# Kernel optimization log

Hardware: AMD Instinct MI355X
Metric: run time of the kernel (lower is better)

## Reference

```python
import jax, jax.numpy as jnp
from jax import lax
import numpy as np

B, DIM, NH, H, W = 4, 256, 8, 32, 32
HEAD_DIM = DIM // NH          # 32
KEY_DIM = HEAD_DIM // 2       # attn_ratio = 0.5 -> 16
QKV_OUT = DIM + 2 * NH * KEY_DIM  # 512
SCALE = KEY_DIM ** -0.5


def setup_inputs() -> dict:
    key = jax.random.key(0)
    ks = jax.random.split(key, 11)
    w = lambda k, shape, s=0.05: jax.random.normal(k, shape, jnp.float32) * s
    return {
        "x": jax.random.normal(ks[0], (B, DIM, H, W), jnp.float32),
        "qkv_w": w(ks[1], (QKV_OUT, DIM)),
        "qkv_b": w(ks[2], (QKV_OUT,)),
        "proj_w": w(ks[3], (DIM, DIM)),
        "proj_b": w(ks[4], (DIM,)),
        "pe_w": w(ks[5], (DIM, 1, 3, 3)),
        "pe_b": w(ks[6], (DIM,)),
        "g1_w": w(ks[7], (DIM // 2, DIM)),
        "g1_b": w(ks[8], (DIM // 2,)),
        "g2_w": w(ks[9], (1, DIM // 2)),
        "g2_b": w(ks[10], (1,)),
    }


def conv1x1(x, w, b):
    # fused Conv2d(1x1, bias=False)+BN -> pointwise matmul + bias
    return jnp.einsum('bchw,oc->bohw', x, w) + b[None, :, None, None]


def reference(x, qkv_w, qkv_b, proj_w, proj_b, pe_w, pe_b, g1_w, g1_b, g2_w, g2_b):
    Bx, C, Hh, Ww = x.shape
    N = Hh * Ww
    qkv = conv1x1(x, qkv_w, qkv_b).reshape(Bx, NH, 2 * KEY_DIM + HEAD_DIM, N)
    q = qkv[:, :, :KEY_DIM]                   # [B, nh, key_dim, N]
    k = qkv[:, :, KEY_DIM:2 * KEY_DIM]        # [B, nh, key_dim, N]
    v = qkv[:, :, 2 * KEY_DIM:]               # [B, nh, head_dim, N]

    # attn = q^T @ k * scale  -> [B, nh, N, N]
    attn = jnp.einsum('bhdn,bhdm->bhnm', q, k) * SCALE

    # learned gate -> scalar dynamic k = floor(N * mean(sigmoid(...)))
    g = jax.nn.sigmoid(conv1x1(jax.nn.relu(conv1x1(x, g1_w, g1_b)), g2_w, g2_b))
    dyn_k = jnp.floor(N * jnp.mean(g)).astype(jnp.int32)

    # rank-based top-k mask (jit-friendly equivalent of topk+scatter):
    # keep entries whose descending rank along the last dim is < dyn_k
    order = jnp.argsort(-attn, axis=-1)       # positions sorted by score desc
    ranks = jnp.argsort(order, axis=-1)       # rank of each position
    attn = jnp.where(ranks < dyn_k, attn, -jnp.inf)
    attn = jax.nn.softmax(attn, axis=-1)

    out = jnp.einsum('bhdn,bhmn->bhdm', v, attn).reshape(Bx, C, Hh, Ww)

    # depthwise 3x3 positional-encoding conv on v reshaped to the image grid
    v_img = v.reshape(Bx, C, Hh, Ww)
    pe = lax.conv_general_dilated(
        v_img, pe_w, window_strides=(1, 1), padding=((1, 1), (1, 1)),
        dimension_numbers=('NCHW', 'OIHW', 'NCHW'), feature_group_count=C,
    ) + pe_b[None, :, None, None]

    return conv1x1(out + pe, proj_w, proj_b)
```

## Files before the change

### kernel.cpp

```cpp
#include <hip/hip_runtime.h>
#include <math.h>

#define NTOK 1024
#define CAP 64

#define LDS_FENCE() asm volatile("s_waitcnt lgkmcnt(0)" ::: "memory")

typedef __bf16 bf16x8 __attribute__((ext_vector_type(8)));
typedef unsigned short u16x8 __attribute__((ext_vector_type(8)));
typedef unsigned short u16x4 __attribute__((ext_vector_type(4)));
typedef float f32x4 __attribute__((ext_vector_type(4)));

__device__ __forceinline__ unsigned short f2bf(float f) {
  unsigned int u = __float_as_uint(f);
  return (unsigned short)((u + 0x7fffu + ((u >> 16) & 1u)) >> 16);
}


template<int OC, int OCB, int P, bool RELU, bool VCAST>
__device__ __forceinline__ void conv_body(const float* __restrict__ in,
    const float* __restrict__ w, const float* __restrict__ bias, float* __restrict__ out,
    unsigned short* __restrict__ vbf, int bid, int tid) {
  constexpr int PB = NTOK / (256 * P);
  const int pb = bid % PB; bid /= PB;
  const int ocb = bid % (OC / OCB); const int b = bid / (OC / OCB);
  const int p0 = pb * 256 * P + tid * P;
  const float* inb = in + (size_t)b * 256 * NTOK + p0;
  const float* wrow = w + (size_t)ocb * OCB * 256;

  float acc[OCB][P];
  #pragma unroll
  for (int j = 0; j < OCB; j++)
    #pragma unroll
    for (int i = 0; i < P; i++) acc[j][i] = 0.f;

  #pragma unroll 2
  for (int c0 = 0; c0 < 256; c0 += 4) {
    float4 wl[OCB];
    #pragma unroll
    for (int j = 0; j < OCB; j++) wl[j] = *(const float4*)&wrow[j * 256 + c0];
    #pragma unroll
    for (int cc = 0; cc < 4; cc++) {
      float xr[P];
      if constexpr (P == 4) {
        float4 t = *(const float4*)&inb[(size_t)(c0 + cc) * NTOK];
        xr[0] = t.x; xr[1] = t.y; xr[2] = t.z; xr[3] = t.w;
      } else if constexpr (P == 2) {
        float2 t = *(const float2*)&inb[(size_t)(c0 + cc) * NTOK];
        xr[0] = t.x; xr[1] = t.y;
      } else {
        xr[0] = inb[(size_t)(c0 + cc) * NTOK];
      }
      #pragma unroll
      for (int j = 0; j < OCB; j++) {
        const float wjc = ((const float*)&wl[j])[cc];
        #pragma unroll
        for (int i = 0; i < P; i++) acc[j][i] = fmaf(wjc, xr[i], acc[j][i]);
      }
    }
  }
  #pragma unroll
  for (int j = 0; j < OCB; j++) {
    const int oc = ocb * OCB + j;
    const float bv = bias[oc];
    float r[P];
    #pragma unroll
    for (int i = 0; i < P; i++) {
      float v = acc[j][i] + bv;
      if (RELU) v = fmaxf(v, 0.f);
      r[i] = v;
    }
    float* op = out + ((size_t)b * OC + oc) * NTOK + p0;
    if constexpr (P == 4) *(float4*)op = make_float4(r[0], r[1], r[2], r[3]);
    else if constexpr (P == 2) *(float2*)op = make_float2(r[0], r[1]);
    else *op = r[0];
    if constexpr (VCAST) {
      if ((oc & 63) >= 32) {
        const int c = (oc >> 6) * 32 + (oc & 63) - 32;
        unsigned short* vp = vbf + ((size_t)b * 256 + c) * NTOK + p0;
        #pragma unroll
        for (int i = 0; i < P; i++) vp[i] = f2bf(r[i]);
      }
    }
  }
}

template<int OC, int OCB, int P, bool RELU, bool VCAST>
__global__ __launch_bounds__(256) void conv1x1_kernel(const float* __restrict__ in,
    const float* __restrict__ w, const float* __restrict__ bias, float* __restrict__ out,
    unsigned short* __restrict__ vbf) {
  conv_body<OC, OCB, P, RELU, VCAST>(in, w, bias, out, vbf, blockIdx.x, threadIdx.x);
}

__global__ __launch_bounds__(256) void qkv_gate1_kernel(const float* __restrict__ x,
    const float* __restrict__ qkv_w, const float* __restrict__ qkv_b, float* __restrict__ qkvb,
    unsigned short* __restrict__ vbf,
    const float* __restrict__ g1_w, const float* __restrict__ g1_b, float* __restrict__ gx) {
  const int bid = blockIdx.x;
  if (bid < 512)
    conv_body<512, 8, 2, false, true>(x, qkv_w, qkv_b, qkvb, vbf, bid, threadIdx.x);
  else
    conv_body<128, 8, 2, true, false>(x, g1_w, g1_b, gx, nullptr, bid - 512, threadIdx.x);
}

__global__ __launch_bounds__(256) void gate2_kernel(const float* __restrict__ gx,
    const float* __restrict__ g2_w, const float* __restrict__ g2_b, double* __restrict__ part) {
  const int idx = blockIdx.x * 256 + threadIdx.x;
  const int b = idx >> 10, p = idx & 1023;
  float acc = g2_b[0];
  const float* gb = gx + (size_t)b * 128 * NTOK + p;
  #pragma unroll 4
  for (int j = 0; j < 128; j++) acc = fmaf(g2_w[j], gb[(size_t)j * NTOK], acc);
  float g = 1.f / (1.f + expf(-acc));
  __shared__ double red[256];
  red[threadIdx.x] = (double)g;
  __syncthreads();
  for (int s = 128; s > 0; s >>= 1) {
    if (threadIdx.x < s) red[threadIdx.x] += red[threadIdx.x + s];
    __syncthreads();
  }
  if (threadIdx.x == 0) part[blockIdx.x] = red[0];
}

__global__ __launch_bounds__(512) void attn_kernel(const float* __restrict__ qkv,
    const unsigned short* __restrict__ vbf,
    const double* __restrict__ part, float* __restrict__ out_attn) {
  const int tid = threadIdx.x;
  const int lane = tid & 63, wv = tid >> 6;
  int bid = blockIdx.x;
  const int mb = bid & 127; bid >>= 7;
  const int h = bid & 7; const int b = bid >> 3;

  double dsum = 0.0;
  #pragma unroll
  for (int i = 0; i < 16; i++) dsum += part[i];
  int dk = (int)floor(1024.0 * (dsum / 4096.0));
  const int dyn_k = dk < 1 ? 1 : (dk > NTOK ? NTOK : dk);

  const float* base = qkv + (size_t)(b * 512 + h * 64) * NTOK;

  __shared__ union RowU { float f[1028]; unsigned short pa[1032]; } rows[8];
  __shared__ float invs[8];
  __shared__ union UU {
    struct {
      int hist[8][64];
      int cnt[8];
      float Bv[8]; int Bn[8];
      struct { float v; int n; } cand[8][CAP];
    } sel;
    float pvred[2][4][8][17];
  } u;

  {
    const float2* k2 = (const float2*)(base + 16 * NTOK);
    const float* qb = base + mb * 8;
    float a0[8], a1[8];
    #pragma unroll
    for (int r = 0; r < 8; r++) { a0[r] = 0.f; a1[r] = 0.f; }
    #pragma unroll
    for (int d = 0; d < 16; d++) {
      float2 kk = k2[d * 512 + tid];
      #pragma unroll
      for (int r = 0; r < 8; r++) {
        const float qv = qb[(size_t)d * NTOK + r];
        a0[r] = fmaf(qv, kk.x, a0[r]);
        a1[r] = fmaf(qv, kk.y, a1[r]);
      }
    }
    #pragma unroll
    for (int r = 0; r < 8; r++)
      ((float2*)rows[r].f)[tid] = make_float2(a0[r] * 0.25f, a1[r] * 0.25f);
  }
  __syncthreads();

  {
    const int r = wv;
    float* smrow = rows[r].f;
    float v[16];
    {
      float4 f0 = ((const float4*)smrow)[lane];
      float4 f1 = ((const float4*)smrow)[64 + lane];
      float4 f2 = ((const float4*)smrow)[128 + lane];
      float4 f3 = ((const float4*)smrow)[192 + lane];
      v[0]=f0.x; v[1]=f0.y; v[2]=f0.z; v[3]=f0.w;
      v[4]=f1.x; v[5]=f1.y; v[6]=f1.z; v[7]=f1.w;
      v[8]=f2.x; v[9]=f2.y; v[10]=f2.z; v[11]=f2.w;
      v[12]=f3.x; v[13]=f3.y; v[14]=f3.z; v[15]=f3.w;
    }
    float mn = v[0], mx = v[0];
    #pragma unroll
    for (int i = 1; i < 16; i++) { mn = fminf(mn, v[i]); mx = fmaxf(mx, v[i]); }
    #pragma unroll
    for (int off = 32; off > 0; off >>= 1) {
      mn = fminf(mn, __shfl_xor(mn, off));
      mx = fmaxf(mx, __shfl_xor(mx, off));
    }

    unsigned int keepmask = 0xFFFFu;
    if (dyn_k < NTOK) {
      float Bv = mx; int Bn = dyn_k - 1;
      const float range = mx - mn;
      const bool fine = (range > 0.f);
      int m = 0;
      if (fine) {
        const float s1 = 64.0f / range;
        u.sel.hist[wv][lane] = 0;
        LDS_FENCE();
        int idx1[16];
        #pragma unroll
        for (int i = 0; i < 16; i++) {
          int ix = (int)((v[i] - mn) * s1);
          ix = ix < 0 ? 0 : (ix > 63 ? 63 : ix);
          idx1[i] = ix;
          atomicAdd(&u.sel.hist[wv][ix], 1);
        }
        LDS_FENCE();
        int cum = u.sel.hist[wv][lane];
        #pragma unroll
        for (int off = 1; off < 64; off <<= 1) {
          int o = __shfl_down(cum, off);
          if (lane + off < 64) cum += o;
        }
        int cumNext = __shfl_down(cum, 1);
        if (lane == 63) cumNext = 0;
        unsigned long long bal = __ballot(cum >= dyn_k && cumNext < dyn_k);
        const int t = (int)__builtin_ctzll(bal);
        const int k2 = dyn_k - __shfl(cumNext, t);
        const float binw = range * (1.0f / 64.0f);
        const float lo = mn + (float)t * binw;
        float s2 = 4096.0f / range;
        if (!(s2 < 3.0e38f)) s2 = 0.f;
        u.sel.hist[wv][lane] = 0;
        LDS_FENCE();
        #pragma unroll
        for (int i = 0; i < 16; i++) {
          if (idx1[i] == t) {
            int ix = (int)((v[i] - lo) * s2);
            ix = ix < 0 ? 0 : (ix > 63 ? 63 : ix);
            atomicAdd(&u.sel.hist[wv][ix], 1);
          }
        }
        LDS_FENCE();
        cum = u.sel.hist[wv][lane];
        #pragma unroll
        for (int off = 1; off < 64; off <<= 1) {
          int o = __shfl_down(cum, off);
          if (lane + off < 64) cum += o;
        }
        cumNext = __shfl_down(cum, 1);
        if (lane == 63) cumNext = 0;
        bal = __ballot(cum >= k2 && cumNext < k2);
        const int t2 = (int)__builtin_ctzll(bal);
        const int k3 = k2 - __shfl(cumNext, t2);
        if (lane == 0) u.sel.cnt[wv] = 0;
        LDS_FENCE();
        #pragma unroll
        for (int i = 0; i < 16; i++) {
          if (idx1[i] == t) {
            int ix = (int)((v[i] - lo) * s2);
            ix = ix < 0 ? 0 : (ix > 63 ? 63 : ix);
            if (ix == t2) {
              int p = atomicAdd(&u.sel.cnt[wv], 1);
              if (p < CAP) { u.sel.cand[wv][p].v = v[i]; u.sel.cand[wv][p].n = (i >> 2) * 256 + lane * 4 + (i & 3); }
            }
          }
        }
        LDS_FENCE();
        m = u.sel.cnt[wv];
        if (m <= CAP) {
          for (int ii = lane; ii < m; ii += 64) {
            float cv = u.sel.cand[wv][ii].v; int cn = u.sel.cand[wv][ii].n;
            int rk = 0;
            for (int j = 0; j < m; j++) {
              float ov = u.sel.cand[wv][j].v; int on = u.sel.cand[wv][j].n;
              rk += ((ov > cv) || (ov == cv && on < cn)) ? 1 : 0;
            }
            if (rk == k3 - 1) { u.sel.Bv[wv] = cv; u.sel.Bn[wv] = cn; }
          }
          LDS_FENCE();
          Bv = u.sel.Bv[wv]; Bn = u.sel.Bn[wv];
        }
      }
      if (fine && m > CAP) {
        keepmask = 0u;
        #pragma unroll
        for (int i = 0; i < 16; i++) {
          const int n_i = (i >> 2) * 256 + lane * 4 + (i & 3);
          const float vi = v[i];
          int rk = 0;
          for (int j = 0; j < NTOK; j++) {
            float ov = smrow[j];
            rk += ((ov > vi) || (ov == vi && j < n_i)) ? 1 : 0;
          }
          if (rk < dyn_k) keepmask |= (1u << i);
        }
      } else {
        keepmask = 0u;
        #pragma unroll
        for (int i = 0; i < 16; i++) {
          const int n_i = (i >> 2) * 256 + lane * 4 + (i & 3);
          if ((v[i] > Bv) || (v[i] == Bv && n_i <= Bn)) keepmask |= (1u << i);
        }
      }
    }
    float e[16]; float s = 0.f;
    #pragma unroll
    for (int i = 0; i < 16; i++) {
      e[i] = ((keepmask >> i) & 1u) ? __expf(v[i] - mx) : 0.f;
      s += e[i];
    }
    #pragma unroll
    for (int off = 32; off > 0; off >>= 1) s += __shfl_xor(s, off);
    if (lane == 0) invs[r] = 1.f / s;
    #pragma unroll
    for (int j = 0; j < 4; j++) {
      u16x4 w4 = { f2bf(e[4*j]), f2bf(e[4*j+1]), f2bf(e[4*j+2]), f2bf(e[4*j+3]) };
      *(u16x4*)&rows[r].pa[j * 256 + lane * 4] = w4;
    }
  }
  __syncthreads();

  {
    const int g = lane >> 4;
    const int m16 = lane & 15;
    const int ksl = wv & 3, dt = wv >> 2;
    const unsigned short* vrow = vbf + ((size_t)(b * 256 + h * 32 + dt * 16 + m16)) * NTOK;
    const unsigned short* parow = rows[lane & 7].pa;
    f32x4 acc = {0.f, 0.f, 0.f, 0.f};
    const int nb = ksl * 256;
    #pragma unroll
    for (int ks = 0; ks < 8; ks++) {
      const int n0 = nb + ks * 32 + g * 8;
      bf16x8 a  = __builtin_bit_cast(bf16x8, *(const u16x8*)&parow[n0]);
      bf16x8 b0 = __builtin_bit_cast(bf16x8, *(const u16x8*)&vrow[n0]);
      acc = __builtin_amdgcn_mfma_f32_16x16x32_bf16(a, b0, acc, 0, 0, 0);
    }
    if (g < 2) {
      #pragma unroll
      for (int q = 0; q < 4; q++)
        u.pvred[dt][ksl][g * 4 + q][m16] = acc[q];
    }
  }
  __syncthreads();
  if (tid < 256) {
    const int r2 = tid & 7, d2 = tid >> 3;
    const int dt = d2 >> 4, m16 = d2 & 15;
    float s = u.pvred[dt][0][r2][m16] + u.pvred[dt][1][r2][m16]
            + u.pvred[dt][2][r2][m16] + u.pvred[dt][3][r2][m16];
    s *= invs[r2];
    out_attn[(size_t)(b * 256 + h * 32 + d2) * NTOK + mb * 8 + r2] = s;
  }
}

__global__ __launch_bounds__(256) void pe_kernel(const float* __restrict__ qkv,
    const float* __restrict__ oattn, const float* __restrict__ pe_w,
    const float* __restrict__ pe_b, float* __restrict__ tmp) {
  int bid = blockIdx.x;
  const int c = bid & 255; const int b = bid >> 8;
  const int oc = ((c >> 5) * 64) + 32 + (c & 31);
  const float* vimg = qkv + (size_t)(b * 512 + oc) * NTOK;
  float wloc[9];
  #pragma unroll
  for (int i = 0; i < 9; i++) wloc[i] = pe_w[c * 9 + i];
  const float bv = pe_b[c];
  const int t = threadIdx.x;
  const int p0 = t * 4;
  const int y = p0 >> 5, x0 = p0 & 31;
  float win[3][6];
  #pragma unroll
  for (int dy = -1; dy <= 1; dy++) {
    const int yy = y + dy;
    float* wr = win[dy + 1];
    if (yy < 0 || yy > 31) {
      #pragma unroll
      for (int i = 0; i < 6; i++) wr[i] = 0.f;
    } else {
      const float* vr = vimg + yy * 32;
      wr[0] = (x0 > 0) ? vr[x0 - 1] : 0.f;
      const float4 mid = *(const float4*)&vr[x0];
      wr[1] = mid.x; wr[2] = mid.y; wr[3] = mid.z; wr[4] = mid.w;
      wr[5] = (x0 < 28) ? vr[x0 + 4] : 0.f;
    }
  }
  const float4 oa = *(const float4*)(oattn + (size_t)(b * 256 + c) * NTOK + p0);
  float r[4];
  #pragma unroll
  for (int i = 0; i < 4; i++) {
    float s = bv;
    #pragma unroll
    for (int dy = 0; dy < 3; dy++) {
      s = fmaf(wloc[dy * 3 + 0], win[dy][i], s);
      s = fmaf(wloc[dy * 3 + 1], win[dy][i + 1], s);
      s = fmaf(wloc[dy * 3 + 2], win[dy][i + 2], s);
    }
    r[i] = s;
  }
  float4 o = make_float4(r[0] + oa.x, r[1] + oa.y, r[2] + oa.z, r[3] + oa.w);
  *(float4*)(tmp + (size_t)(b * 256 + c) * NTOK + p0) = o;
}

extern "C" void kernel_launch(void* const* d_in, const int* in_sizes, int n_in,
                              void* d_out, int out_size, void* d_ws, size_t ws_size,
                              hipStream_t stream) {
  const float* x      = (const float*)d_in[0];
  const float* qkv_w  = (const float*)d_in[1];
  const float* qkv_b  = (const float*)d_in[2];
  const float* proj_w = (const float*)d_in[3];
  const float* proj_b = (const float*)d_in[4];
  const float* pe_w   = (const float*)d_in[5];
  const float* pe_b   = (const float*)d_in[6];
  const float* g1_w   = (const float*)d_in[7];
  const float* g1_b   = (const float*)d_in[8];
  const float* g2_w   = (const float*)d_in[9];
  const float* g2_b   = (const float*)d_in[10];
  float* out = (float*)d_out;

  char* ws = (char*)d_ws;
  float*  qkvb  = (float*)(ws);
  float*  oattn = (float*)(ws + (8u << 20));
  float*  tmp   = (float*)(ws + (12u << 20));
  unsigned short* vbf = (unsigned short*)(ws + (12u << 20));
  float*  gx    = (float*)(ws + (16u << 20));
  double* part  = (double*)(ws + (18u << 20));

  qkv_gate1_kernel<<<640, 256, 0, stream>>>(x, qkv_w, qkv_b, qkvb, vbf, g1_w, g1_b, gx);
  gate2_kernel<<<16, 256, 0, stream>>>(gx, g2_w, g2_b, part);
  attn_kernel<<<4096, 512, 0, stream>>>(qkvb, vbf, part, oattn);
  pe_kernel<<<1024, 256, 0, stream>>>(qkvb, oattn, pe_w, pe_b, tmp);
  conv1x1_kernel<256, 4, 2, false, false><<<512, 256, 0, stream>>>(tmp, proj_w, proj_b, out, nullptr);
}
```

Measured before the change: 147.1 us.

## Parallelize gate reduction across more blocks and precompute dyn_k once

The gate second-layer conv now runs on 256 blocks instead of 16. Each block has 16 thread groups splitting the 128-channel dot product, with a shared-memory reduction that writes per-pixel sigmoid values. A new single-block kernel sums these in double and writes the clamped dyn_k, so each attention block reads one int instead of summing 16 partials. The projection conv tile configuration also changes from OCB=4,P=2 to OCB=8,P=1. This adds a kernel launch in exchange for more parallelism in a tiny serial-ish stage.

```diff
diff --git a/kernel.cpp b/kernel.cpp
--- a/kernel.cpp
+++ b/kernel.cpp
@@ -104,38 +104,53 @@
 }
 
 __global__ __launch_bounds__(256) void gate2_kernel(const float* __restrict__ gx,
-    const float* __restrict__ g2_w, const float* __restrict__ g2_b, double* __restrict__ part) {
-  const int idx = blockIdx.x * 256 + threadIdx.x;
-  const int b = idx >> 10, p = idx & 1023;
-  float acc = g2_b[0];
-  const float* gb = gx + (size_t)b * 128 * NTOK + p;
-  #pragma unroll 4
-  for (int j = 0; j < 128; j++) acc = fmaf(g2_w[j], gb[(size_t)j * NTOK], acc);
-  float g = 1.f / (1.f + expf(-acc));
+    const float* __restrict__ g2_w, const float* __restrict__ g2_b, float* __restrict__ gvals) {
+  const int tid = threadIdx.x;
+  const int p_l = tid & 15, jg = tid >> 4;
+  const int gp = blockIdx.x * 16 + p_l;
+  const int b = gp >> 10, p = gp & 1023;
+  float s = 0.f;
+  const float* gb = gx + ((size_t)b * 128 + jg * 8) * NTOK + p;
+  #pragma unroll
+  for (int jj = 0; jj < 8; jj++) s = fmaf(g2_w[jg * 8 + jj], gb[(size_t)jj * NTOK], s);
+  __shared__ float red[16][17];
+  red[jg][p_l] = s;
+  __syncthreads();
+  if (tid < 16) {
+    float a = g2_b[0];
+    #pragma unroll
+    for (int g = 0; g < 16; g++) a += red[g][tid];
+    gvals[blockIdx.x * 16 + tid] = 1.f / (1.f + expf(-a));
+  }
+}
+
+__global__ void dynk_kernel(const float* __restrict__ gvals, int* __restrict__ dynk) {
+  const int t = threadIdx.x;
+  double s = 0.0;
+  #pragma unroll
+  for (int i = 0; i < 16; i++) s += (double)gvals[t + 256 * i];
   __shared__ double red[256];
-  red[threadIdx.x] = (double)g;
+  red[t] = s;
   __syncthreads();
-  for (int s = 128; s > 0; s >>= 1) {
-    if (threadIdx.x < s) red[threadIdx.x] += red[threadIdx.x + s];
+  for (int st = 128; st > 0; st >>= 1) {
+    if (t < st) red[t] += red[t + st];
     __syncthreads();
   }
-  if (threadIdx.x == 0) part[blockIdx.x] = red[0];
+  if (t == 0) {
+    int k = (int)floor(1024.0 * (red[0] / 4096.0));
+    *dynk = k < 1 ? 1 : (k > NTOK ? NTOK : k);
+  }
 }
 
 __global__ __launch_bounds__(512) void attn_kernel(const float* __restrict__ qkv,
     const unsigned short* __restrict__ vbf,
-    const double* __restrict__ part, float* __restrict__ out_attn) {
+    const int* __restrict__ dynk_p, float* __restrict__ out_attn) {
   const int tid = threadIdx.x;
   const int lane = tid & 63, wv = tid >> 6;
   int bid = blockIdx.x;
   const int mb = bid & 127; bid >>= 7;
   const int h = bid & 7; const int b = bid >> 3;
-
-  double dsum = 0.0;
-  #pragma unroll
-  for (int i = 0; i < 16; i++) dsum += part[i];
-  int dk = (int)floor(1024.0 * (dsum / 4096.0));
-  const int dyn_k = dk < 1 ? 1 : (dk > NTOK ? NTOK : dk);
+  const int dyn_k = *dynk_p;
 
   const float* base = qkv + (size_t)(b * 512 + h * 64) * NTOK;
 
@@ -421,11 +436,13 @@
   float*  tmp   = (float*)(ws + (12u << 20));
   unsigned short* vbf = (unsigned short*)(ws + (12u << 20));
   float*  gx    = (float*)(ws + (16u << 20));
-  double* part  = (double*)(ws + (18u << 20));
+  float*  gvals = (float*)(ws + (18u << 20));
+  int*    dynk  = (int*)(ws + (18u << 20) + (64u << 10));
 
   qkv_gate1_kernel<<<640, 256, 0, stream>>>(x, qkv_w, qkv_b, qkvb, vbf, g1_w, g1_b, gx);
-  gate2_kernel<<<16, 256, 0, stream>>>(gx, g2_w, g2_b, part);
-  attn_kernel<<<4096, 512, 0, stream>>>(qkvb, vbf, part, oattn);
+  gate2_kernel<<<256, 256, 0, stream>>>(gx, g2_w, g2_b, gvals);
+  dynk_kernel<<<1, 256, 0, stream>>>(gvals, dynk);
+  attn_kernel<<<4096, 512, 0, stream>>>(qkvb, vbf, dynk, oattn);
   pe_kernel<<<1024, 256, 0, stream>>>(qkvb, oattn, pe_w, pe_b, tmp);
-  conv1x1_kernel<256, 4, 2, false, false><<<512, 256, 0, stream>>>(tmp, proj_w, proj_b, out, nullptr);
-}
+  conv1x1_kernel<256, 8, 1, false, false><<<512, 256, 0, stream>>>(tmp, proj_w, proj_b, out, nullptr);
+}
```

After: 141.5 us (median of 2 runs). 1.04x faster.
